# Kernel tuning notes

Measured on AMD Instinct MI355X. Metric: run time of the kernel, lower is better.

Reference implementation:

```python
import jax, jax.numpy as jnp
import numpy as np

NEG_SLOPE = 0.2
N_NODES = 100000
N_EDGES = 3200000
F_IN = 256
H1, D1 = 8, 8          # layer-1 heads / per-head dim (num_hidden=8)
N_CLASSES = 40         # output layer: 1 head, 40 classes


def gat_conv(x, W, attn_l, attn_r, b, src, dst, activation):
    """DGL GATConv (no dropout, no residual).
    x: [N, F_in], W: [F_in, H*D], attn_l/attn_r: [H, D], b: [H*D].
    Returns [N, H, D].
    """
    N = x.shape[0]
    H, D = attn_l.shape
    feat = (x @ W).reshape(N, H, D)                       # [N,H,D]
    el = jnp.sum(feat * attn_l, axis=-1)                  # [N,H]
    er = jnp.sum(feat * attn_r, axis=-1)                  # [N,H]
    e = jax.nn.leaky_relu(el[src] + er[dst], NEG_SLOPE)   # [E,H] edge scores
    # segment softmax over incoming edges of each dst node
    m = jax.ops.segment_max(e, dst, num_segments=N)       # [N,H]
    ex = jnp.exp(e - m[dst])                              # [E,H]
    s = jax.ops.segment_sum(ex, dst, num_segments=N)      # [N,H]
    alpha = ex / s[dst]                                   # [E,H]
    # weighted gather-scatter aggregation
    out = jax.ops.segment_sum(feat[src] * alpha[:, :, None], dst,
                              num_segments=N)             # [N,H,D]
    out = out + b.reshape(H, D)
    if activation is not None:
        out = activation(out)
    return out


def setup_inputs() -> dict:
    key = jax.random.key(0)
    ks = jax.random.split(key, 12)
    x = jax.random.normal(ks[0], (N_NODES, F_IN), dtype=jnp.float32)
    src = jax.random.randint(ks[1], (N_EDGES,), 0, N_NODES)
    dst = jax.random.randint(ks[2], (N_EDGES,), 0, N_NODES)
    s1 = 1.0 / np.sqrt(F_IN)
    s2 = 1.0 / np.sqrt(H1 * D1)
    W1 = jax.random.normal(ks[3], (F_IN, H1 * D1), jnp.float32) * s1
    attn_l1 = jax.random.normal(ks[4], (H1, D1), jnp.float32) * s2
    attn_r1 = jax.random.normal(ks[5], (H1, D1), jnp.float32) * s2
    b1 = jnp.zeros((H1 * D1,), jnp.float32)
    W2 = jax.random.normal(ks[6], (H1 * D1, 1 * N_CLASSES), jnp.float32) * s2
    attn_l2 = jax.random.normal(ks[7], (1, N_CLASSES), jnp.float32) * 0.1
    attn_r2 = jax.random.normal(ks[8], (1, N_CLASSES), jnp.float32) * 0.1
    b2 = jnp.zeros((N_CLASSES,), jnp.float32)
    return {"x": x, "W1": W1, "attn_l1": attn_l1, "attn_r1": attn_r1, "b1": b1,
            "W2": W2, "attn_l2": attn_l2, "attn_r2": attn_r2, "b2": b2,
            "src": src, "dst": dst}


def reference(x, W1, attn_l1, attn_r1, b1, W2, attn_l2, attn_r2, b2, src, dst):
    h = gat_conv(x, W1, attn_l1, attn_r1, b1, src, dst, jax.nn.relu)
    h = h.reshape(h.shape[0], -1)                         # flatten(1) -> [N, H1*D1]
    logits = gat_conv(h, W2, attn_l2, attn_r2, b2, src, dst, None)
    return logits.mean(axis=1)                            # mean over 1 out-head -> [N, C]
```

## Files before the change

kernel.cpp:

```cpp
#include <hip/hip_runtime.h>
#include <hip/hip_fp16.h>
#include <math.h>

#define NN 100000
#define NE 3200000
#define FIN 256
#define NEG 0.2f
#define BSH 7
#define NB  782
#define EPB 4096
#define NBLK 782
#define CAPB 8192
#define DCAP 64

typedef _Float16 h8 __attribute__((ext_vector_type(8)));
typedef float f32x4 __attribute__((ext_vector_type(4)));

__global__ __launch_bounds__(256) void k_w1h(const float* __restrict__ W1,
                                             __half* __restrict__ w1frag) {
  int f = blockIdx.x * 256 + threadIdx.x;
  int j = f & 7;
  int lane = (f >> 3) & 63;
  int g = f >> 9;
  int ks = g & 7, ct = g >> 3;
  int k = ks * 32 + ((lane >> 4) & 3) * 8 + j;
  int c = ct * 16 + (lane & 15);
  w1frag[f] = __float2half(W1[k * 64 + c]);
}

__global__ __launch_bounds__(256) void k_gemm1(
    const float* __restrict__ x, const __half* __restrict__ w1frag,
    __half* __restrict__ feat1h) {
  const int lane = threadIdx.x & 63;
  const int wave = threadIdx.x >> 6;
  const int rowBase = blockIdx.x * 64 + wave * 16;
  const int arow = rowBase + (lane & 15);
  const int kc = lane >> 4;
  const bool act = (arow < NN);
  f32x4 acc0 = {0.f,0.f,0.f,0.f}, acc1 = {0.f,0.f,0.f,0.f};
  f32x4 acc2 = {0.f,0.f,0.f,0.f}, acc3 = {0.f,0.f,0.f,0.f};
  const float4* __restrict__ x4 = reinterpret_cast<const float4*>(x);
  const h8* __restrict__ wf = reinterpret_cast<const h8*>(w1frag);
#pragma unroll
  for (int ks = 0; ks < 8; ++ks) {
    h8 a;
    if (act) {
      float4 xa = x4[(size_t)arow * 64 + ks * 8 + kc * 2];
      float4 xb = x4[(size_t)arow * 64 + ks * 8 + kc * 2 + 1];
      a[0] = (_Float16)xa.x; a[1] = (_Float16)xa.y;
      a[2] = (_Float16)xa.z; a[3] = (_Float16)xa.w;
      a[4] = (_Float16)xb.x; a[5] = (_Float16)xb.y;
      a[6] = (_Float16)xb.z; a[7] = (_Float16)xb.w;
    } else {
#pragma unroll
      for (int j = 0; j < 8; ++j) a[j] = (_Float16)0.f;
    }
    h8 b0 = wf[(0 * 8 + ks) * 64 + lane];
    h8 b1 = wf[(1 * 8 + ks) * 64 + lane];
    h8 b2 = wf[(2 * 8 + ks) * 64 + lane];
    h8 b3 = wf[(3 * 8 + ks) * 64 + lane];
    acc0 = __builtin_amdgcn_mfma_f32_16x16x32_f16(a, b0, acc0, 0, 0, 0);
    acc1 = __builtin_amdgcn_mfma_f32_16x16x32_f16(a, b1, acc1, 0, 0, 0);
    acc2 = __builtin_amdgcn_mfma_f32_16x16x32_f16(a, b2, acc2, 0, 0, 0);
    acc3 = __builtin_amdgcn_mfma_f32_16x16x32_f16(a, b3, acc3, 0, 0, 0);
  }
  const int crow = rowBase + (lane >> 4) * 4;
  const int ccol = lane & 15;
#pragma unroll
  for (int r = 0; r < 4; ++r) {
    int row = crow + r;
    if (row < NN) {
      __half* fr = feat1h + (size_t)row * 64 + ccol;
      fr[0]  = __float2half(acc0[r]);
      fr[16] = __float2half(acc1[r]);
      fr[32] = __float2half(acc2[r]);
      fr[48] = __float2half(acc3[r]);
    }
  }
}

__global__ __launch_bounds__(256) void k_el1(
    const __half* __restrict__ feat1h, const float* __restrict__ al1,
    const float* __restrict__ ar1, float* __restrict__ el1, float* __restrict__ er1) {
  const int g = blockIdx.x * 256 + threadIdx.x;
  const int n = g >> 3, h = g & 7;
  uint4 rv = *reinterpret_cast<const uint4*>(feat1h + (size_t)n * 64 + h * 8);
  float f[8];
  {
    unsigned w0 = rv.x, w1 = rv.y, w2 = rv.z, w3 = rv.w;
    float2 f0 = __half22float2(*reinterpret_cast<__half2*>(&w0));
    float2 f1 = __half22float2(*reinterpret_cast<__half2*>(&w1));
    float2 f2 = __half22float2(*reinterpret_cast<__half2*>(&w2));
    float2 f3 = __half22float2(*reinterpret_cast<__half2*>(&w3));
    f[0]=f0.x; f[1]=f0.y; f[2]=f1.x; f[3]=f1.y;
    f[4]=f2.x; f[5]=f2.y; f[6]=f3.x; f[7]=f3.y;
  }
  float pl = 0.f, pr = 0.f;
#pragma unroll
  for (int j = 0; j < 8; ++j) {
    pl = fmaf(f[j], al1[h * 8 + j], pl);
    pr = fmaf(f[j], ar1[h * 8 + j], pr);
  }
  el1[g] = pl;
  er1[g] = pr;
}

__global__ __launch_bounds__(256) void k_hist(const int* __restrict__ dst,
                                              int* __restrict__ bcnt) {
  __shared__ int lcnt[1024];
  for (int i = threadIdx.x; i < 1024; i += 256) lcnt[i] = 0;
  __syncthreads();
  const int base = blockIdx.x * EPB;
  const int n = min(EPB, NE - base);
  for (int k = threadIdx.x; k < n; k += 256)
    atomicAdd(&lcnt[dst[base + k] >> BSH], 1);
  __syncthreads();
  for (int i = threadIdx.x; i < NB; i += 256)
    if (lcnt[i]) atomicAdd(&bcnt[i], lcnt[i]);
}

__global__ __launch_bounds__(256) void k_bscan(const int* __restrict__ bcnt,
    int* __restrict__ bbase, int* __restrict__ cursor) {
  __shared__ int part[256];
  const int t = threadIdx.x;
  int v[4]; int s = 0;
#pragma unroll
  for (int j = 0; j < 4; ++j) { int i = t*4+j; v[j] = (i < NB) ? bcnt[i] : 0; s += v[j]; }
  part[t] = s; __syncthreads();
  for (int off = 1; off < 256; off <<= 1) {
    int a = (t >= off) ? part[t-off] : 0;
    __syncthreads(); part[t] += a; __syncthreads();
  }
  int excl = (t > 0) ? part[t-1] : 0;
#pragma unroll
  for (int j = 0; j < 4; ++j) {
    int i = t*4+j;
    if (i < NB) { bbase[i] = excl; cursor[i] = excl; }
    excl += v[j];
  }
  if (t == 255) bbase[NB] = part[255];
}

__global__ __launch_bounds__(256) void k_binA(const int* __restrict__ src,
    const int* __restrict__ dst, int* __restrict__ cursor, int* __restrict__ pairs) {
  __shared__ int cnt[1024];
  __shared__ int lstart[1024];
  __shared__ int gbase[1024];
  __shared__ int lcur[1024];
  __shared__ int part[256];
  __shared__ int pack[EPB];
  __shared__ unsigned short bof[EPB];
  const int t = threadIdx.x;
  const int base = blockIdx.x * EPB;
  const int n = min(EPB, NE - base);
  for (int i = t; i < 1024; i += 256) { cnt[i] = 0; lcur[i] = 0; }
  __syncthreads();
  for (int k = t; k < n; k += 256) atomicAdd(&cnt[dst[base+k] >> BSH], 1);
  __syncthreads();
  int v[4]; int s = 0;
#pragma unroll
  for (int j = 0; j < 4; ++j) { v[j] = cnt[t*4+j]; s += v[j]; }
  part[t] = s; __syncthreads();
  for (int off = 1; off < 256; off <<= 1) {
    int a = (t >= off) ? part[t-off] : 0;
    __syncthreads(); part[t] += a; __syncthreads();
  }
  int excl = (t > 0) ? part[t-1] : 0;
#pragma unroll
  for (int j = 0; j < 4; ++j) { lstart[t*4+j] = excl; excl += v[j]; }
  __syncthreads();
  for (int b = t; b < NB; b += 256)
    if (cnt[b]) gbase[b] = atomicAdd(&cursor[b], cnt[b]);
  __syncthreads();
  for (int k = t; k < n; k += 256) {
    int d = dst[base+k];
    int b = d >> BSH;
    int pos = lstart[b] + atomicAdd(&lcur[b], 1);
    pack[pos] = src[base+k] | ((d & 127) << 20);
    bof[pos]  = (unsigned short)b;
  }
  __syncthreads();
  for (int i = t; i < n; i += 256) {
    int b = bof[i];
    pairs[gbase[b] + (i - lstart[b])] = pack[i];
  }
}

__global__ __launch_bounds__(256) void k_binB(const int* __restrict__ bbase,
    const int* __restrict__ pairs, int* __restrict__ csr,
    int* __restrict__ offs, int* __restrict__ deg) {
  __shared__ int hist[128];
  __shared__ int incl[128];
  __shared__ int lcur[128];
  __shared__ int out[CAPB];
  const int b = blockIdx.x;
  const int t = threadIdx.x;
  const int lo = bbase[b], hi = bbase[b+1];
  const int n = hi - lo;
  if (t < 128) { hist[t] = 0; lcur[t] = 0; }
  __syncthreads();
  for (int k = t; k < n; k += 256) atomicAdd(&hist[(pairs[lo+k] >> 20) & 127], 1);
  __syncthreads();
  if (t < 128) incl[t] = hist[t];
  __syncthreads();
  for (int off = 1; off < 128; off <<= 1) {
    int a = (t < 128 && t >= off) ? incl[t-off] : 0;
    __syncthreads();
    if (t < 128) incl[t] += a;
    __syncthreads();
  }
  if (t < 128) {
    int gnode = b*128 + t;
    if (gnode < NN) {
      offs[gnode] = lo + ((t > 0) ? incl[t-1] : 0);
      deg[gnode]  = hist[t];
    }
  }
  __syncthreads();
  for (int k = t; k < n; k += 256) {
    int v = pairs[lo+k];
    int node = (v >> 20) & 127;
    int e = (node > 0) ? incl[node-1] : 0;
    int pos = e + atomicAdd(&lcur[node], 1);
    if (pos < CAPB) out[pos] = v & 0xFFFFF;
  }
  __syncthreads();
  for (int i = t; i < n && i < CAPB; i += 256) csr[lo+i] = out[i];
}

__global__ __launch_bounds__(64) void k_agg1(
    const __half* __restrict__ feat1h, const float* __restrict__ el1,
    const float* __restrict__ er1, const float* __restrict__ b1,
    const int* __restrict__ offs, const int* __restrict__ deg,
    const int* __restrict__ csr_src, float* __restrict__ h1) {
  const int d = blockIdx.x;
  const int lane = threadIdx.x;
  const int e8 = lane >> 3;
  const int h  = lane & 7;
  const int off = offs[d];
  const int n = deg[d];
  const float erd = er1[d*8 + h];
  int sAll = (lane < n) ? csr_src[off + lane] : 0;
  float ss = 0.f;
  float ac[8];
#pragma unroll
  for (int k = 0; k < 8; ++k) ac[k] = 0.f;
#pragma unroll 2
  for (int j0 = 0; j0 < n; j0 += 8) {
    const int j = j0 + e8;
    const bool act = (j < n);
    const int sreg = __shfl(sAll, j & 63);
    int s;
    if (j0 + 7 < 64) s = sreg;
    else s = act ? ((j < 64) ? sreg : csr_src[off + j]) : 0;
    float elv = act ? el1[s*8 + h] : 0.f;
    float t = elv + erd;
    float e = (t > 0.f) ? t : NEG * t;
    float p = act ? __expf(e) : 0.f;
    uint4 rv = make_uint4(0u,0u,0u,0u);
    if (act) rv = *reinterpret_cast<const uint4*>(feat1h + (size_t)s*64 + h*8);
    float f[8];
    {
      unsigned w0 = rv.x, w1 = rv.y, w2 = rv.z, w3 = rv.w;
      float2 f0 = __half22float2(*reinterpret_cast<__half2*>(&w0));
      float2 f1 = __half22float2(*reinterpret_cast<__half2*>(&w1));
      float2 f2 = __half22float2(*reinterpret_cast<__half2*>(&w2));
      float2 f3 = __half22float2(*reinterpret_cast<__half2*>(&w3));
      f[0]=f0.x; f[1]=f0.y; f[2]=f1.x; f[3]=f1.y;
      f[4]=f2.x; f[5]=f2.y; f[6]=f3.x; f[7]=f3.y;
    }
    ss += p;
#pragma unroll
    for (int k = 0; k < 8; ++k) ac[k] = fmaf(p, f[k], ac[k]);
  }
#pragma unroll
  for (int msk = 8; msk < 64; msk <<= 1) {
    ss += __shfl_xor(ss, msk);
#pragma unroll
    for (int k = 0; k < 8; ++k) ac[k] += __shfl_xor(ac[k], msk);
  }
  if (e8 == 0) {
    float invS = (ss > 0.f) ? 1.f / ss : 0.f;
    float o[8];
#pragma unroll
    for (int k = 0; k < 8; ++k) {
      float v = ac[k] * invS + b1[h*8 + k];
      o[k] = (v > 0.f) ? v : 0.f;
    }
    float4* p4 = reinterpret_cast<float4*>(h1 + (size_t)d*64 + h*8);
    p4[0] = make_float4(o[0], o[1], o[2], o[3]);
    p4[1] = make_float4(o[4], o[5], o[6], o[7]);
  }
}

__global__ __launch_bounds__(64) void k_gemm2(
    const float* __restrict__ h1, const float* __restrict__ W2,
    const float* __restrict__ al2, const float* __restrict__ ar2,
    __half* __restrict__ feat2h, float* __restrict__ el2, float* __restrict__ er2) {
  const int n = blockIdx.x;
  const int c = threadIdx.x;
  const float* __restrict__ hr = h1 + (size_t)n*64;
  float acc = 0.f;
  if (c < 40) {
    for (int k = 0; k < 64; ++k)
      acc = fmaf(hr[k], W2[k*40 + c], acc);
    feat2h[(size_t)n*40 + c] = __float2half(acc);
  }
  float pl = (c < 40) ? acc * al2[c] : 0.f;
  float pr = (c < 40) ? acc * ar2[c] : 0.f;
#pragma unroll
  for (int msk = 32; msk >= 1; msk >>= 1) {
    pl += __shfl_xor(pl, msk);
    pr += __shfl_xor(pr, msk);
  }
  if (c == 0) { el2[n] = pl; er2[n] = pr; }
}

__global__ __launch_bounds__(64) void k_agg2(
    const __half* __restrict__ feat2h, const float* __restrict__ el2,
    const float* __restrict__ er2, const float* __restrict__ b2,
    const int* __restrict__ offs, const int* __restrict__ deg,
    const int* __restrict__ csr_src, float* __restrict__ out) {
  __shared__ float red[64][8];
  __shared__ float sca[DCAP];
  const int d = blockIdx.x;
  const int lane = threadIdx.x;
  const int off = offs[d];
  const int n = deg[d];
  const float erd = er2[d];
  int sAll = 0;
  float ssum = 0.f;
  for (int j = lane; j < n; j += 64) {
    int s = csr_src[off + j];
    if (j < 64) sAll = s;
    float t = el2[s] + erd;
    float e = (t > 0.f) ? t : NEG * t;
    float p = __expf(e);
    if (j < DCAP) sca[j] = p;
    ssum += p;
  }
#pragma unroll
  for (int msk = 1; msk < 64; msk <<= 1) ssum += __shfl_xor(ssum, msk);
  const float invS = (ssum > 0.f) ? 1.f / ssum : 0.f;
  __syncthreads();
  for (int j = lane; j < n && j < DCAP; j += 64)
    sca[j] *= invS;
  __syncthreads();
  const int e = lane / 5;
  const int q = lane % 5;
  const bool lact = (lane < 60);
  float acc[8];
#pragma unroll
  for (int k = 0; k < 8; ++k) acc[k] = 0.f;
  for (int j0 = 0; j0 < n; j0 += 12) {
    const int j = j0 + e;
    const bool act = lact && (j < n);
    const int sreg = __shfl(sAll, j & 63);
    int s = 0;
    float a = 0.f;
    if (act) {
      if (j < 64) { s = sreg; a = sca[j]; }
      else {
        s = csr_src[off + j];
        float t = el2[s] + erd;
        float ee = (t > 0.f) ? t : NEG * t;
        a = __expf(ee) * invS;
      }
    }
    uint4 rv = make_uint4(0u,0u,0u,0u);
    if (act) rv = *reinterpret_cast<const uint4*>(feat2h + (size_t)s*40 + q*8);
    float f[8];
    {
      unsigned w0 = rv.x, w1 = rv.y, w2 = rv.z, w3 = rv.w;
      float2 f0 = __half22float2(*reinterpret_cast<__half2*>(&w0));
      float2 f1 = __half22float2(*reinterpret_cast<__half2*>(&w1));
      float2 f2 = __half22float2(*reinterpret_cast<__half2*>(&w2));
      float2 f3 = __half22float2(*reinterpret_cast<__half2*>(&w3));
      f[0]=f0.x; f[1]=f0.y; f[2]=f1.x; f[3]=f1.y;
      f[4]=f2.x; f[5]=f2.y; f[6]=f3.x; f[7]=f3.y;
    }
#pragma unroll
    for (int k = 0; k < 8; ++k) acc[k] = fmaf(a, f[k], acc[k]);
  }
#pragma unroll
  for (int k = 0; k < 8; ++k) red[lane][k] = acc[k];
  __syncthreads();
  if (lane < 40) {
    const int qq = lane >> 3;
    const int kk = lane & 7;
    float sum = 0.f;
#pragma unroll
    for (int ee = 0; ee < 12; ++ee) sum += red[5*ee + qq][kk];
    out[(size_t)d*40 + lane] = sum + b2[lane];
  }
}

extern "C" void kernel_launch(void* const* d_in, const int* in_sizes, int n_in,
                              void* d_out, int out_size, void* d_ws, size_t ws_size,
                              hipStream_t stream) {
  const float* x   = (const float*)d_in[0];
  const float* W1  = (const float*)d_in[1];
  const float* al1 = (const float*)d_in[2];
  const float* ar1 = (const float*)d_in[3];
  const float* b1  = (const float*)d_in[4];
  const float* W2  = (const float*)d_in[5];
  const float* al2 = (const float*)d_in[6];
  const float* ar2 = (const float*)d_in[7];
  const float* b2  = (const float*)d_in[8];
  const int* src   = (const int*)d_in[9];
  const int* dst   = (const int*)d_in[10];
  float* out = (float*)d_out;

  char* ws = (char*)d_ws;
  size_t o = 0;
  auto alloc = [&](size_t bytes) -> void* {
    o = (o + 255) & ~(size_t)255;
    void* p = ws + o;
    o += bytes;
    return p;
  };
  __half* feat1h = (__half*)alloc((size_t)NN * 64 * 2);
  float*  el1    = (float*)alloc((size_t)NN * 8 * 4);
  float*  er1    = (float*)alloc((size_t)NN * 8 * 4);
  float*  h1     = (float*)alloc((size_t)NN * 64 * 4);
  int*    bcnt   = (int*)alloc((size_t)(NB) * 4);
  int*    bbase  = (int*)alloc((size_t)(NB+1) * 4);
  int*    cursor = (int*)alloc((size_t)NB * 4);
  int*    offs   = (int*)alloc((size_t)NN * 4);
  int*    deg    = (int*)alloc((size_t)NN * 4);
  int*    pairs  = (int*)alloc((size_t)NE * 4);
  int*    csr    = (int*)alloc((size_t)NE * 4);
  __half* w1frag = (__half*)alloc((size_t)16384 * 2);
  __half* feat2h = (__half*)feat1h;
  float*  el2    = el1;
  float*  er2    = er1;

  hipMemsetAsync(bcnt, 0, (size_t)NB * 4, stream);

  k_w1h  <<<64, 256, 0, stream>>>(W1, w1frag);
  k_gemm1<<<(NN + 63) / 64, 256, 0, stream>>>(x, w1frag, feat1h);
  k_el1  <<<3125, 256, 0, stream>>>(feat1h, al1, ar1, el1, er1);
  k_hist <<<NBLK, 256, 0, stream>>>(dst, bcnt);
  k_bscan<<<1, 256, 0, stream>>>(bcnt, bbase, cursor);
  k_binA <<<NBLK, 256, 0, stream>>>(src, dst, cursor, pairs);
  k_binB <<<NB, 256, 0, stream>>>(bbase, pairs, csr, offs, deg);
  k_agg1 <<<NN, 64, 0, stream>>>(feat1h, el1, er1, b1, offs, deg, csr, h1);
  k_gemm2<<<NN, 64, 0, stream>>>(h1, W2, al2, ar2, feat2h, el2, er2);
  k_agg2 <<<NN, 64, 0, stream>>>(feat2h, el2, er2, b2, offs, deg, csr, out);
}
```

Baseline: 333.3 us.

## Recompute source attention scores from gathered features instead of separate el gathers

Drops the precomputed el1/el2 arrays and recomputes each edge's source score as a dot product with attn_l on the feature row already gathered during aggregation. This removes one random gather per edge per head. Layer 2 is restructured to match layer 1's single-pass 8-lanes-per-edge scheme, with feat2 padded to a 64-half stride, a shuffle reduction for the score, and no shared-memory prepass or block sync. The cost is extra FMAs and shuffles per edge, lanes 5-7 of each group of eight sitting idle in layer 2, and el now computed from fp16 features.

```diff
diff --git a/kernel.cpp b/kernel.cpp
--- a/kernel.cpp
+++ b/kernel.cpp
@@ -11,7 +11,6 @@
 #define EPB 4096
 #define NBLK 782
 #define CAPB 8192
-#define DCAP 64
 
 typedef _Float16 h8 __attribute__((ext_vector_type(8)));
 typedef float f32x4 __attribute__((ext_vector_type(4)));
@@ -79,9 +78,9 @@
   }
 }
 
-__global__ __launch_bounds__(256) void k_el1(
-    const __half* __restrict__ feat1h, const float* __restrict__ al1,
-    const float* __restrict__ ar1, float* __restrict__ el1, float* __restrict__ er1) {
+__global__ __launch_bounds__(256) void k_er1(
+    const __half* __restrict__ feat1h, const float* __restrict__ ar1,
+    float* __restrict__ er1) {
   const int g = blockIdx.x * 256 + threadIdx.x;
   const int n = g >> 3, h = g & 7;
   uint4 rv = *reinterpret_cast<const uint4*>(feat1h + (size_t)n * 64 + h * 8);
@@ -95,13 +94,9 @@
     f[0]=f0.x; f[1]=f0.y; f[2]=f1.x; f[3]=f1.y;
     f[4]=f2.x; f[5]=f2.y; f[6]=f3.x; f[7]=f3.y;
   }
-  float pl = 0.f, pr = 0.f;
-#pragma unroll
-  for (int j = 0; j < 8; ++j) {
-    pl = fmaf(f[j], al1[h * 8 + j], pl);
-    pr = fmaf(f[j], ar1[h * 8 + j], pr);
-  }
-  el1[g] = pl;
+  float pr = 0.f;
+#pragma unroll
+  for (int j = 0; j < 8; ++j) pr = fmaf(f[j], ar1[h * 8 + j], pr);
   er1[g] = pr;
 }
 
@@ -229,7 +224,7 @@
 }
 
 __global__ __launch_bounds__(64) void k_agg1(
-    const __half* __restrict__ feat1h, const float* __restrict__ el1,
+    const __half* __restrict__ feat1h, const float* __restrict__ al1,
     const float* __restrict__ er1, const float* __restrict__ b1,
     const int* __restrict__ offs, const int* __restrict__ deg,
     const int* __restrict__ csr_src, float* __restrict__ h1) {
@@ -240,6 +235,9 @@
   const int off = offs[d];
   const int n = deg[d];
   const float erd = er1[d*8 + h];
+  float a1[8];
+#pragma unroll
+  for (int k = 0; k < 8; ++k) a1[k] = al1[h*8 + k];
   int sAll = (lane < n) ? csr_src[off + lane] : 0;
   float ss = 0.f;
   float ac[8];
@@ -253,10 +251,6 @@
     int s;
     if (j0 + 7 < 64) s = sreg;
     else s = act ? ((j < 64) ? sreg : csr_src[off + j]) : 0;
-    float elv = act ? el1[s*8 + h] : 0.f;
-    float t = elv + erd;
-    float e = (t > 0.f) ? t : NEG * t;
-    float p = act ? __expf(e) : 0.f;
     uint4 rv = make_uint4(0u,0u,0u,0u);
     if (act) rv = *reinterpret_cast<const uint4*>(feat1h + (size_t)s*64 + h*8);
     float f[8];
@@ -269,6 +263,12 @@
       f[0]=f0.x; f[1]=f0.y; f[2]=f1.x; f[3]=f1.y;
       f[4]=f2.x; f[5]=f2.y; f[6]=f3.x; f[7]=f3.y;
     }
+    float elv = 0.f;
+#pragma unroll
+    for (int k = 0; k < 8; ++k) elv = fmaf(f[k], a1[k], elv);
+    float t = elv + erd;
+    float e = (t > 0.f) ? t : NEG * t;
+    float p = act ? __expf(e) : 0.f;
     ss += p;
 #pragma unroll
     for (int k = 0; k < 8; ++k) ac[k] = fmaf(p, f[k], ac[k]);
@@ -295,8 +295,8 @@
 
 __global__ __launch_bounds__(64) void k_gemm2(
     const float* __restrict__ h1, const float* __restrict__ W2,
-    const float* __restrict__ al2, const float* __restrict__ ar2,
-    __half* __restrict__ feat2h, float* __restrict__ el2, float* __restrict__ er2) {
+    const float* __restrict__ ar2,
+    __half* __restrict__ feat2p, float* __restrict__ er2) {
   const int n = blockIdx.x;
   const int c = threadIdx.x;
   const float* __restrict__ hr = h1 + (size_t)n*64;
@@ -304,71 +304,45 @@
   if (c < 40) {
     for (int k = 0; k < 64; ++k)
       acc = fmaf(hr[k], W2[k*40 + c], acc);
-    feat2h[(size_t)n*40 + c] = __float2half(acc);
-  }
-  float pl = (c < 40) ? acc * al2[c] : 0.f;
+    feat2p[(size_t)n*64 + c] = __float2half(acc);
+  }
   float pr = (c < 40) ? acc * ar2[c] : 0.f;
 #pragma unroll
-  for (int msk = 32; msk >= 1; msk >>= 1) {
-    pl += __shfl_xor(pl, msk);
-    pr += __shfl_xor(pr, msk);
-  }
-  if (c == 0) { el2[n] = pl; er2[n] = pr; }
+  for (int msk = 32; msk >= 1; msk >>= 1) pr += __shfl_xor(pr, msk);
+  if (c == 0) er2[n] = pr;
 }
 
 __global__ __launch_bounds__(64) void k_agg2(
-    const __half* __restrict__ feat2h, const float* __restrict__ el2,
+    const __half* __restrict__ feat2p, const float* __restrict__ al2,
     const float* __restrict__ er2, const float* __restrict__ b2,
     const int* __restrict__ offs, const int* __restrict__ deg,
     const int* __restrict__ csr_src, float* __restrict__ out) {
-  __shared__ float red[64][8];
-  __shared__ float sca[DCAP];
   const int d = blockIdx.x;
   const int lane = threadIdx.x;
+  const int e8 = lane >> 3;
+  const int q8 = lane & 7;
+  const bool real = (q8 < 5);
   const int off = offs[d];
   const int n = deg[d];
   const float erd = er2[d];
-  int sAll = 0;
-  float ssum = 0.f;
-  for (int j = lane; j < n; j += 64) {
-    int s = csr_src[off + j];
-    if (j < 64) sAll = s;
-    float t = el2[s] + erd;
-    float e = (t > 0.f) ? t : NEG * t;
-    float p = __expf(e);
-    if (j < DCAP) sca[j] = p;
-    ssum += p;
-  }
-#pragma unroll
-  for (int msk = 1; msk < 64; msk <<= 1) ssum += __shfl_xor(ssum, msk);
-  const float invS = (ssum > 0.f) ? 1.f / ssum : 0.f;
-  __syncthreads();
-  for (int j = lane; j < n && j < DCAP; j += 64)
-    sca[j] *= invS;
-  __syncthreads();
-  const int e = lane / 5;
-  const int q = lane % 5;
-  const bool lact = (lane < 60);
-  float acc[8];
-#pragma unroll
-  for (int k = 0; k < 8; ++k) acc[k] = 0.f;
-  for (int j0 = 0; j0 < n; j0 += 12) {
-    const int j = j0 + e;
-    const bool act = lact && (j < n);
+  float a2[8];
+#pragma unroll
+  for (int k = 0; k < 8; ++k) a2[k] = real ? al2[q8*8 + k] : 0.f;
+  int sAll = (lane < n) ? csr_src[off + lane] : 0;
+  float ss = 0.f;
+  float ac[8];
+#pragma unroll
+  for (int k = 0; k < 8; ++k) ac[k] = 0.f;
+#pragma unroll 2
+  for (int j0 = 0; j0 < n; j0 += 8) {
+    const int j = j0 + e8;
+    const bool act = (j < n);
     const int sreg = __shfl(sAll, j & 63);
-    int s = 0;
-    float a = 0.f;
-    if (act) {
-      if (j < 64) { s = sreg; a = sca[j]; }
-      else {
-        s = csr_src[off + j];
-        float t = el2[s] + erd;
-        float ee = (t > 0.f) ? t : NEG * t;
-        a = __expf(ee) * invS;
-      }
-    }
+    int s;
+    if (j0 + 7 < 64) s = sreg;
+    else s = act ? ((j < 64) ? sreg : csr_src[off + j]) : 0;
     uint4 rv = make_uint4(0u,0u,0u,0u);
-    if (act) rv = *reinterpret_cast<const uint4*>(feat2h + (size_t)s*40 + q*8);
+    if (act && real) rv = *reinterpret_cast<const uint4*>(feat2p + (size_t)s*64 + q8*8);
     float f[8];
     {
       unsigned w0 = rv.x, w1 = rv.y, w2 = rv.z, w3 = rv.w;
@@ -379,19 +353,33 @@
       f[0]=f0.x; f[1]=f0.y; f[2]=f1.x; f[3]=f1.y;
       f[4]=f2.x; f[5]=f2.y; f[6]=f3.x; f[7]=f3.y;
     }
-#pragma unroll
-    for (int k = 0; k < 8; ++k) acc[k] = fmaf(a, f[k], acc[k]);
-  }
-#pragma unroll
-  for (int k = 0; k < 8; ++k) red[lane][k] = acc[k];
-  __syncthreads();
-  if (lane < 40) {
-    const int qq = lane >> 3;
-    const int kk = lane & 7;
-    float sum = 0.f;
-#pragma unroll
-    for (int ee = 0; ee < 12; ++ee) sum += red[5*ee + qq][kk];
-    out[(size_t)d*40 + lane] = sum + b2[lane];
+    float ep = 0.f;
+#pragma unroll
+    for (int k = 0; k < 8; ++k) ep = fmaf(f[k], a2[k], ep);
+    ep += __shfl_xor(ep, 1);
+    ep += __shfl_xor(ep, 2);
+    ep += __shfl_xor(ep, 4);
+    float t = ep + erd;
+    float e = (t > 0.f) ? t : NEG * t;
+    float p = act ? __expf(e) : 0.f;
+    ss += p;
+#pragma unroll
+    for (int k = 0; k < 8; ++k) ac[k] = fmaf(p, f[k], ac[k]);
+  }
+#pragma unroll
+  for (int msk = 8; msk < 64; msk <<= 1) {
+    ss += __shfl_xor(ss, msk);
+#pragma unroll
+    for (int k = 0; k < 8; ++k) ac[k] += __shfl_xor(ac[k], msk);
+  }
+  if (e8 == 0 && real) {
+    float invS = (ss > 0.f) ? 1.f / ss : 0.f;
+    float o[8];
+#pragma unroll
+    for (int k = 0; k < 8; ++k) o[k] = ac[k] * invS + b2[q8*8 + k];
+    float* po = out + (size_t)d*40 + q8*8;
+#pragma unroll
+    for (int k = 0; k < 8; ++k) po[k] = o[k];
   }
 }
 
@@ -420,7 +408,6 @@
     return p;
   };
   __half* feat1h = (__half*)alloc((size_t)NN * 64 * 2);
-  float*  el1    = (float*)alloc((size_t)NN * 8 * 4);
   float*  er1    = (float*)alloc((size_t)NN * 8 * 4);
   float*  h1     = (float*)alloc((size_t)NN * 64 * 4);
   int*    bcnt   = (int*)alloc((size_t)(NB) * 4);
@@ -431,20 +418,19 @@
   int*    pairs  = (int*)alloc((size_t)NE * 4);
   int*    csr    = (int*)alloc((size_t)NE * 4);
   __half* w1frag = (__half*)alloc((size_t)16384 * 2);
-  __half* feat2h = (__half*)feat1h;
-  float*  el2    = el1;
+  __half* feat2p = (__half*)feat1h;
   float*  er2    = er1;
 
   hipMemsetAsync(bcnt, 0, (size_t)NB * 4, stream);
 
   k_w1h  <<<64, 256, 0, stream>>>(W1, w1frag);
   k_gemm1<<<(NN + 63) / 64, 256, 0, stream>>>(x, w1frag, feat1h);
-  k_el1  <<<3125, 256, 0, stream>>>(feat1h, al1, ar1, el1, er1);
+  k_er1  <<<3125, 256, 0, stream>>>(feat1h, ar1, er1);
   k_hist <<<NBLK, 256, 0, stream>>>(dst, bcnt);
   k_bscan<<<1, 256, 0, stream>>>(bcnt, bbase, cursor);
   k_binA <<<NBLK, 256, 0, stream>>>(src, dst, cursor, pairs);
   k_binB <<<NB, 256, 0, stream>>>(bbase, pairs, csr, offs, deg);
-  k_agg1 <<<NN, 64, 0, stream>>>(feat1h, el1, er1, b1, offs, deg, csr, h1);
-  k_gemm2<<<NN, 64, 0, stream>>>(h1, W2, al2, ar2, feat2h, el2, er2);
-  k_agg2 <<<NN, 64, 0, stream>>>(feat2h, el2, er2, b2, offs, deg, csr, out);
-}
+  k_agg1 <<<NN, 64, 0, stream>>>(feat1h, al1, er1, b1, offs, deg, csr, h1);
+  k_gemm2<<<NN, 64, 0, stream>>>(h1, W2, ar2, feat2p, er2);
+  k_agg2 <<<NN, 64, 0, stream>>>(feat2p, al2, er2, b2, offs, deg, csr, out);
+}
```

Measured after the change: 303.6 us. -8.9%, faster.
